# Kernel tuning notes

Measured on AMD Instinct MI355X. Metric: run time of the kernel, lower is better.

The kernel has to match this reference:

```python
import jax, jax.numpy as jnp
import numpy as np

B, N, CIN, C = 2, 400000, 192, 128
Y, X, Z = 512, 512, 40
EPS1 = 1e-5   # default BatchNorm1d eps for feature_proj
EPS2 = 1e-3   # norm_fn eps=0.001 for shared_conv BN


def setup_inputs() -> dict:
    key = jax.random.key(0)
    ks = jax.random.split(key, 12)
    voxel_features = jax.random.normal(ks[0], (N, CIN), jnp.float32)
    bi = jax.random.randint(ks[1], (N,), 0, B)
    zi = jax.random.randint(ks[2], (N,), 0, Z)
    yi = jax.random.randint(ks[3], (N,), 0, Y)
    xi = jax.random.randint(ks[4], (N,), 0, X)
    voxel_coords = jnp.stack([bi, zi, yi, xi], axis=1).astype(jnp.int32)  # (N,4)=[b,z,y,x]
    # feature_proj: Linear(CIN->C) + BN1d (inference stats) + ReLU
    W_proj = jax.random.normal(ks[5], (CIN, C), jnp.float32) * np.float32(1.0 / np.sqrt(CIN))
    b_proj = jnp.zeros((C,), jnp.float32)
    bn1_gamma = jnp.ones((C,), jnp.float32)
    bn1_beta = jnp.zeros((C,), jnp.float32)
    bn1_mean = jax.random.normal(ks[6], (C,), jnp.float32) * np.float32(0.1)
    bn1_var = jax.random.uniform(ks[7], (C,), jnp.float32, 0.5, 1.5)
    # shared_conv: SubMConv2d(C,C,3,pad=1,bias) + BN(eps=1e-3) + ReLU
    conv_w = jax.random.normal(ks[8], (3, 3, C, C), jnp.float32) * np.float32(1.0 / np.sqrt(9 * C))
    conv_b = jnp.zeros((C,), jnp.float32)
    bn2_gamma = jnp.ones((C,), jnp.float32)
    bn2_beta = jnp.zeros((C,), jnp.float32)
    bn2_mean = jax.random.normal(ks[9], (C,), jnp.float32) * np.float32(0.1)
    bn2_var = jax.random.uniform(ks[10], (C,), jnp.float32, 0.5, 1.5)
    return dict(voxel_features=voxel_features, voxel_coords=voxel_coords,
                W_proj=W_proj, b_proj=b_proj,
                bn1_gamma=bn1_gamma, bn1_beta=bn1_beta, bn1_mean=bn1_mean, bn1_var=bn1_var,
                conv_w=conv_w, conv_b=conv_b,
                bn2_gamma=bn2_gamma, bn2_beta=bn2_beta, bn2_mean=bn2_mean, bn2_var=bn2_var)


def reference(voxel_features, voxel_coords, W_proj, b_proj,
              bn1_gamma, bn1_beta, bn1_mean, bn1_var,
              conv_w, conv_b, bn2_gamma, bn2_beta, bn2_mean, bn2_var):
    # 1) feature_proj (Linear + BN1d inference + ReLU)
    f = voxel_features @ W_proj + b_proj                      # (N, C)
    f = (f - bn1_mean) * jax.lax.rsqrt(bn1_var + EPS1) * bn1_gamma + bn1_beta
    f = jax.nn.relu(f)
    # 2) bev_aggregate: unique([b,y,x]) + index_add == scatter-sum to dense BEV grid
    bi, yi, xi = voxel_coords[:, 0], voxel_coords[:, 2], voxel_coords[:, 3]
    dense = jnp.zeros((B, Y, X, C), f.dtype).at[bi, yi, xi].add(f)
    active = jnp.zeros((B, Y, X), bool).at[bi, yi, xi].set(True)
    # 3) SubMConv2d(3x3, pad=1) + BN + ReLU; subm == dense conv masked to active sites
    out = jax.lax.conv_general_dilated(dense, conv_w, (1, 1), 'SAME',
                                       dimension_numbers=('NHWC', 'HWIO', 'NHWC')) + conv_b
    out = (out - bn2_mean) * jax.lax.rsqrt(bn2_var + EPS2) * bn2_gamma + bn2_beta
    out = jax.nn.relu(out)
    # sparse tensor only holds active sites; zero elsewhere
    return jnp.where(active[..., None], out, jnp.float32(0.0))  # (B, Y, X, C)
```

## Files before the change

### kernel.cpp

```cpp
#include <hip/hip_runtime.h>

#define Bq 2
#define Yq 512
#define Xq 512
#define NVOX 400000

typedef __bf16 bf16x8 __attribute__((ext_vector_type(8)));
typedef float f32x4 __attribute__((ext_vector_type(4)));
typedef float f32x16 __attribute__((ext_vector_type(16)));
typedef short s16x8 __attribute__((ext_vector_type(8)));
typedef short s16x2 __attribute__((ext_vector_type(2)));

__device__ __forceinline__ short f2bf_s(float f){
    return __builtin_bit_cast(short, static_cast<__bf16>(f));
}

__device__ __forceinline__ void atomic_pk_add_bf16(short* addr, unsigned data){
#if __has_builtin(__builtin_amdgcn_global_atomic_fadd_v2bf16)
    s16x2 v; v[0] = (short)(data & 0xffff); v[1] = (short)(data >> 16);
    __builtin_amdgcn_global_atomic_fadd_v2bf16(
        (__attribute__((address_space(1))) s16x2*)addr, v);
#else
    asm volatile("global_atomic_pk_add_bf16 %0, %1, off"
                 :: "v"(addr), "v"(data) : "memory");
#endif
}

__global__ void kprep(const float* __restrict__ conv_w, const float* __restrict__ W_proj,
                      short* __restrict__ wR, short* __restrict__ wpT){
    int tid = blockIdx.x*256 + threadIdx.x;
    if (tid < 9*128*128){
        int tap = tid >> 14; int r = tid & 16383; int co = r >> 7; int ci = r & 127;
        int nn = co >> 5, l31 = co & 31;
        int kcc = ci >> 4, hi = (ci >> 3) & 1, j = ci & 7;
        wR[(size_t)tap*16384 + nn*4096 + kcc*512 + (hi*32 + l31)*8 + j] =
            f2bf_s(conv_w[tap*16384 + ci*128 + co]);
    }
    int e = tid - 9*128*128;
    if (e >= 0 && e < 128*192){
        int co = e / 192; int ci = e - co*192;
        wpT[e] = f2bf_s(W_proj[ci*128 + co]);
    }
}

__global__ void kcount(const int* __restrict__ vc, unsigned* __restrict__ cnt,
                       unsigned char* __restrict__ act){
    int i = blockIdx.x*256 + threadIdx.x;
    if (i >= NVOX) return;
    const int4 c = *reinterpret_cast<const int4*>(vc + i*4);
    int cell = (c.x*Yq + c.z)*Xq + c.w;
    act[cell] = 1;
    atomicAdd(&cnt[cell], 1u);
}

__global__ void __launch_bounds__(256, 2)
kproj(const float* __restrict__ vf, const int* __restrict__ vc,
      const unsigned* __restrict__ cnt,
      const short* __restrict__ wpT, const float* __restrict__ bp,
      const float* __restrict__ g1, const float* __restrict__ be1,
      const float* __restrict__ mu1, const float* __restrict__ va1,
      short* __restrict__ dbf){
    __shared__ char smem[64*200*2];
    __shared__ int cellsPk[64];
    short*    A  = (short*)smem;
    unsigned* st = (unsigned*)smem;
    const int t = threadIdx.x;
    const int v0 = blockIdx.x * 64;

    const float4* vf4 = reinterpret_cast<const float4*>(vf);
    #pragma unroll
    for (int j = 0; j < 12; ++j){
        int i = t + j*256;
        int v = i / 48, kq = i - v*48;
        float4 x = vf4[(size_t)(v0 + v)*48 + kq];
        short4 s; s.x=f2bf_s(x.x); s.y=f2bf_s(x.y); s.z=f2bf_s(x.z); s.w=f2bf_s(x.w);
        *reinterpret_cast<short4*>(&A[v*200 + kq*4]) = s;
    }
    if (t < 64){
        int vi = v0 + t;
        int bi = vc[vi*4 + 0], yi = vc[vi*4 + 2], xi = vc[vi*4 + 3];
        unsigned cn = cnt[(bi*Yq + yi)*Xq + xi];
        int P = (bi*514 + (yi + 1))*514 + (xi + 1);
        cellsPk[t] = (P*8 + ((xi + 1) & 7)) | ((cn > 1) ? (1 << 30) : 0);
    }
    __syncthreads();

    const int w  = t >> 6;
    const int l  = t & 63;
    const int lr = l & 15;
    const int q  = l >> 4;

    const short* wp_lane = wpT + (size_t)(w*32 + lr)*192 + q*8;
    bf16x8 bb[2][6];
    #pragma unroll
    for (int n = 0; n < 2; ++n)
        #pragma unroll
        for (int kc = 0; kc < 6; ++kc)
            bb[n][kc] = *reinterpret_cast<const bf16x8*>(wp_lane + n*16*192 + kc*32);

    f32x4 acc[4][2] = {};
    #pragma unroll
    for (int kc = 0; kc < 6; ++kc){
        bf16x8 a[4];
        #pragma unroll
        for (int m = 0; m < 4; ++m)
            a[m] = *reinterpret_cast<const bf16x8*>(&A[(m*16 + lr)*200 + kc*32 + q*8]);
        #pragma unroll
        for (int m = 0; m < 4; ++m)
            #pragma unroll
            for (int n = 0; n < 2; ++n)
                acc[m][n] = __builtin_amdgcn_mfma_f32_16x16x32_bf16(a[m], bb[n][kc], acc[m][n], 0, 0, 0);
    }

    __syncthreads();
    const int odd = lr & 1;
    #pragma unroll
    for (int n = 0; n < 2; ++n){
        int c = w*32 + n*16 + lr;
        float s1  = g1[c] * rsqrtf(va1[c] + 1e-5f);
        float sh1 = be1[c] + (bp[c] - mu1[c]) * s1;
        int jj = w*16 + n*8 + (lr >> 1);
        #pragma unroll
        for (int m = 0; m < 4; ++m){
            #pragma unroll
            for (int r = 0; r < 4; ++r){
                int vx = m*16 + q*4 + r;
                float val = fmaxf(fmaf(acc[m][n][r], s1, sh1), 0.f);
                float vp  = __shfl_xor(val, 1);
                if (!odd){
                    unsigned data = (unsigned)(unsigned short)f2bf_s(val)
                                  | ((unsigned)(unsigned short)f2bf_s(vp) << 16);
                    st[vx*68 + jj] = data;
                }
            }
        }
    }
    __syncthreads();

    unsigned* dbf_u32 = reinterpret_cast<unsigned*>(dbf);
    #pragma unroll
    for (int i = 0; i < 16; ++i){
        int vv = w*16 + i;
        int pk = cellsPk[vv];
        int multi = pk >> 30;
        int P = (pk & 0x3fffffff) >> 3, xp7 = pk & 7;
        unsigned data = st[vv*68 + l];
        size_t idx = (size_t)P*64 + (((l >> 2) ^ xp7) << 2) + (l & 3);
        if (multi){
            if (data) atomic_pk_add_bf16((short*)(dbf_u32 + idx), data);
        } else {
            dbf_u32[idx] = data;
        }
    }
}

__global__ void __launch_bounds__(256, 3)
kconv(const short* __restrict__ dbf, const short* __restrict__ wR,
      const unsigned char* __restrict__ act, const float* __restrict__ cb,
      const float* __restrict__ g2, const float* __restrict__ be2,
      const float* __restrict__ mu2, const float* __restrict__ va2,
      float* __restrict__ out){
    __shared__ short Atile[3*1056*8];
    const int t = threadIdx.x;
    const int bid = (blockIdx.x & 7)*1024 + (blockIdx.x >> 3);
    const int b   = bid >> 12;
    const int rem = bid & 4095;
    const int y   = rem >> 3;
    const int x0  = (rem & 7) << 6;

    const int w   = t >> 6, l = t & 63;
    const int l31 = l & 31, hi = l >> 5;

    #pragma unroll
    for (int j = 0; j < 13; ++j){
        int S = j*256 + t;
        if (S < 3168){
            int r = S / 1056, s = S - r*1056;
            const short* gp = dbf + ((size_t)((b*514 + (y + r))*514 + x0)*16 + s)*8;
            __builtin_amdgcn_global_load_lds(
                (const __attribute__((address_space(1))) void*)gp,
                (__attribute__((address_space(3))) void*)
                    ((char*)Atile + (size_t)(j*256 + w*64)*16), 16, 0, 0);
        }
    }

    const short* wRb = wR + (size_t)w*4096 + l*8;
    bf16x8 Breg[2][8];
    #pragma unroll
    for (int kcc = 0; kcc < 8; ++kcc)
        Breg[0][kcc] = *reinterpret_cast<const bf16x8*>(wRb + kcc*512);

    __syncthreads();

    f32x16 acc[2] = {};

    #pragma unroll
    for (int tp = 0; tp < 9; ++tp){
        if (tp < 8){
            const short* wn = wRb + (size_t)(tp+1)*16384;
            #pragma unroll
            for (int kcc = 0; kcc < 8; ++kcc)
                Breg[(tp+1) & 1][kcc] = *reinterpret_cast<const bf16x8*>(wn + kcc*512);
        }
        const int ky = tp / 3, kx = tp - ky*3;
        const int p0 = l31 + kx, p1 = p0 + 32;
        const int base0 = (ky*1056 + p0*16)*8;
        const int base1 = (ky*1056 + p1*16)*8;
        const int pk7 = p0 & 7;
        #pragma unroll
        for (int kcc = 0; kcc < 8; ++kcc){
            const int ks = (kcc & 3)*2 + hi, hh = kcc >> 2;
            const int q  = ((hh*8 + ks) ^ pk7) << 3;
            bf16x8 a0 = *reinterpret_cast<const bf16x8*>(&Atile[base0 + q]);
            bf16x8 a1 = *reinterpret_cast<const bf16x8*>(&Atile[base1 + q]);
            acc[0] = __builtin_amdgcn_mfma_f32_32x32x16_bf16(a0, Breg[tp & 1][kcc], acc[0], 0, 0, 0);
            acc[1] = __builtin_amdgcn_mfma_f32_32x32x16_bf16(a1, Breg[tp & 1][kcc], acc[1], 0, 0, 0);
        }
    }

    const int c = w*32 + l31;
    const float s2  = g2[c] * rsqrtf(va2[c] + 1e-3f);
    const float sh2 = be2[c] + (cb[c] - mu2[c]) * s2;
    const size_t rowcell = (size_t)(b*Yq + y)*Xq + x0;
    #pragma unroll
    for (int mi = 0; mi < 2; ++mi){
        #pragma unroll
        for (int r = 0; r < 16; ++r){
            int pos = mi*32 + (r & 3) + ((r >> 2) << 3) + hi*4;
            size_t cell = rowcell + pos;
            float v = act[cell] ? fmaxf(fmaf(acc[mi][r], s2, sh2), 0.f) : 0.f;
            out[cell*128 + c] = v;
        }
    }
}

extern "C" void kernel_launch(void* const* d_in, const int* in_sizes, int n_in,
                              void* d_out, int out_size, void* d_ws, size_t ws_size,
                              hipStream_t stream){
    const float* vf  = (const float*)d_in[0];
    const int*   vc  = (const int*)  d_in[1];
    const float* Wp  = (const float*)d_in[2];
    const float* bp  = (const float*)d_in[3];
    const float* g1  = (const float*)d_in[4];
    const float* be1 = (const float*)d_in[5];
    const float* mu1 = (const float*)d_in[6];
    const float* va1 = (const float*)d_in[7];
    const float* cw  = (const float*)d_in[8];
    const float* cb  = (const float*)d_in[9];
    const float* g2  = (const float*)d_in[10];
    const float* be2 = (const float*)d_in[11];
    const float* mu2 = (const float*)d_in[12];
    const float* va2 = (const float*)d_in[13];
    float* out = (float*)d_out;
    char* ws = (char*)d_ws;

    if (ws_size < 138233856ull) return;
    short* dbf = (short*)ws;
    unsigned char* act = (unsigned char*)(ws + 135268352);
    short* wR  = (short*)(ws + 135792640);
    short* wpT = (short*)(ws + 136087552);
    unsigned* cnt = (unsigned*)(ws + 136136704);

    hipMemsetAsync(dbf, 0, 135268352, stream);
    hipMemsetAsync(act, 0, 524288, stream);
    hipMemsetAsync(cnt, 0, 2097152, stream);
    kprep<<<672, 256, 0, stream>>>(cw, Wp, wR, wpT);
    kcount<<<1563, 256, 0, stream>>>(vc, cnt, act);
    kproj<<<6250, 256, 0, stream>>>(vf, vc, cnt, wpT, bp, g1, be1, mu1, va1, dbf);
    kconv<<<8192, 256, 0, stream>>>(dbf, wR, act, cb, g2, be2, mu2, va2, out);
}
```

Measured before the change: 363.2 us.

## Tile conv blocks over two output rows with 2x2 MFMA per wave

Each conv block now covers two output rows by 64 columns and loads a 4-row halo tile instead of a 3-row one, which cuts redundant halo loads from the dense BEV buffer. Each wave handles one row and 64 output channels, so it computes a 2x2 grid of MFMA tiles and reuses every A fragment against two weight banks. Weight banks are double-buffered in registers, with schedule barriers separating the prefetch from the compute. The cost is more registers and LDS per block, so launch bounds drop to 2 blocks per CU, and the grid is halved.

```diff
diff --git a/kernel.cpp b/kernel.cpp
--- a/kernel.cpp
+++ b/kernel.cpp
@@ -31,9 +31,9 @@
     int tid = blockIdx.x*256 + threadIdx.x;
     if (tid < 9*128*128){
         int tap = tid >> 14; int r = tid & 16383; int co = r >> 7; int ci = r & 127;
-        int nn = co >> 5, l31 = co & 31;
+        int g = co >> 5, l31 = co & 31;
         int kcc = ci >> 4, hi = (ci >> 3) & 1, j = ci & 7;
-        wR[(size_t)tap*16384 + nn*4096 + kcc*512 + (hi*32 + l31)*8 + j] =
+        wR[(size_t)tap*16384 + g*4096 + kcc*512 + (hi*32 + l31)*8 + j] =
             f2bf_s(conv_w[tap*16384 + ci*128 + co]);
     }
     int e = tid - 9*128*128;
@@ -154,29 +154,30 @@
     }
 }
 
-__global__ void __launch_bounds__(256, 3)
+__global__ void __launch_bounds__(256, 2)
 kconv(const short* __restrict__ dbf, const short* __restrict__ wR,
       const unsigned char* __restrict__ act, const float* __restrict__ cb,
       const float* __restrict__ g2, const float* __restrict__ be2,
       const float* __restrict__ mu2, const float* __restrict__ va2,
       float* __restrict__ out){
-    __shared__ short Atile[3*1056*8];
+    __shared__ short Atile[4*1056*8];
     const int t = threadIdx.x;
-    const int bid = (blockIdx.x & 7)*1024 + (blockIdx.x >> 3);
-    const int b   = bid >> 12;
-    const int rem = bid & 4095;
-    const int y   = rem >> 3;
+    const int bid = (blockIdx.x & 7)*512 + (blockIdx.x >> 3);
+    const int b   = bid >> 11;
+    const int rem = bid & 2047;
+    const int y0  = (rem >> 3) << 1;
     const int x0  = (rem & 7) << 6;
 
     const int w   = t >> 6, l = t & 63;
+    const int yy  = w >> 1, nn = w & 1;
     const int l31 = l & 31, hi = l >> 5;
 
     #pragma unroll
-    for (int j = 0; j < 13; ++j){
+    for (int j = 0; j < 17; ++j){
         int S = j*256 + t;
-        if (S < 3168){
+        if (S < 4224){
             int r = S / 1056, s = S - r*1056;
-            const short* gp = dbf + ((size_t)((b*514 + (y + r))*514 + x0)*16 + s)*8;
+            const short* gp = dbf + ((size_t)((b*514 + (y0 + r))*514 + x0)*16 + s)*8;
             __builtin_amdgcn_global_load_lds(
                 (const __attribute__((address_space(1))) void*)gp,
                 (__attribute__((address_space(3))) void*)
@@ -184,52 +185,75 @@
         }
     }
 
-    const short* wRb = wR + (size_t)w*4096 + l*8;
-    bf16x8 Breg[2][8];
-    #pragma unroll
-    for (int kcc = 0; kcc < 8; ++kcc)
-        Breg[0][kcc] = *reinterpret_cast<const bf16x8*>(wRb + kcc*512);
-
-    __syncthreads();
-
-    f32x16 acc[2] = {};
+    const short* wR_lane = wR + (size_t)(2*nn)*4096 + l*8;
+
+    bf16x8 BrA[2][8], BrB[2][8];
+
+    #define LOADBANK(DST, TP) do {                                            \
+        const short* g0_ = wR_lane + (size_t)(TP)*16384;                      \
+        _Pragma("unroll")                                                     \
+        for (int kcc_ = 0; kcc_ < 8; ++kcc_){                                 \
+            DST[0][kcc_] = *reinterpret_cast<const bf16x8*>(g0_ + kcc_*512);  \
+            DST[1][kcc_] = *reinterpret_cast<const bf16x8*>(g0_ + 4096 + kcc_*512); \
+        }                                                                     \
+    } while(0)
+
+    #define TAPBODY(BK, TP) do {                                              \
+        const int ky_ = (TP)/3, kx_ = (TP) - ky_*3;                           \
+        const int row_ = yy + ky_;                                            \
+        const int p0_ = l31 + kx_, p1_ = p0_ + 32;                            \
+        const int b0_ = (row_*1056 + p0_*16)*8;                               \
+        const int b1_ = (row_*1056 + p1_*16)*8;                               \
+        const int pk_ = p0_ & 7;                                              \
+        _Pragma("unroll")                                                     \
+        for (int kcc_ = 0; kcc_ < 8; ++kcc_){                                 \
+            const int ks_ = (kcc_ & 3)*2 + hi, hh_ = kcc_ >> 2;               \
+            const int q_  = ((hh_*8 + ks_) ^ pk_) << 3;                       \
+            bf16x8 a0_ = *reinterpret_cast<const bf16x8*>(&Atile[b0_ + q_]);  \
+            bf16x8 a1_ = *reinterpret_cast<const bf16x8*>(&Atile[b1_ + q_]);  \
+            acc[0][0] = __builtin_amdgcn_mfma_f32_32x32x16_bf16(a0_, BK[0][kcc_], acc[0][0], 0, 0, 0); \
+            acc[0][1] = __builtin_amdgcn_mfma_f32_32x32x16_bf16(a0_, BK[1][kcc_], acc[0][1], 0, 0, 0); \
+            acc[1][0] = __builtin_amdgcn_mfma_f32_32x32x16_bf16(a1_, BK[0][kcc_], acc[1][0], 0, 0, 0); \
+            acc[1][1] = __builtin_amdgcn_mfma_f32_32x32x16_bf16(a1_, BK[1][kcc_], acc[1][1], 0, 0, 0); \
+        }                                                                     \
+    } while(0)
+
+    LOADBANK(BrA, 0);
+    __syncthreads();
+
+    f32x16 acc[2][2] = {};
 
     #pragma unroll
     for (int tp = 0; tp < 9; ++tp){
-        if (tp < 8){
-            const short* wn = wRb + (size_t)(tp+1)*16384;
+        if ((tp & 1) == 0){
+            if (tp < 8) LOADBANK(BrB, tp+1);
+            __builtin_amdgcn_sched_barrier(0);
+            TAPBODY(BrA, tp);
+        } else {
+            LOADBANK(BrA, tp+1);
+            __builtin_amdgcn_sched_barrier(0);
+            TAPBODY(BrB, tp);
+        }
+    }
+    #undef TAPBODY
+    #undef LOADBANK
+
+    const int yg = y0 + yy;
+    const size_t rowcell = (size_t)(b*Yq + yg)*Xq + x0;
+    #pragma unroll
+    for (int ni = 0; ni < 2; ++ni){
+        int c = nn*64 + ni*32 + l31;
+        float s2  = g2[c] * rsqrtf(va2[c] + 1e-3f);
+        float sh2 = be2[c] + (cb[c] - mu2[c]) * s2;
+        #pragma unroll
+        for (int mi = 0; mi < 2; ++mi){
             #pragma unroll
-            for (int kcc = 0; kcc < 8; ++kcc)
-                Breg[(tp+1) & 1][kcc] = *reinterpret_cast<const bf16x8*>(wn + kcc*512);
-        }
-        const int ky = tp / 3, kx = tp - ky*3;
-        const int p0 = l31 + kx, p1 = p0 + 32;
-        const int base0 = (ky*1056 + p0*16)*8;
-        const int base1 = (ky*1056 + p1*16)*8;
-        const int pk7 = p0 & 7;
-        #pragma unroll
-        for (int kcc = 0; kcc < 8; ++kcc){
-            const int ks = (kcc & 3)*2 + hi, hh = kcc >> 2;
-            const int q  = ((hh*8 + ks) ^ pk7) << 3;
-            bf16x8 a0 = *reinterpret_cast<const bf16x8*>(&Atile[base0 + q]);
-            bf16x8 a1 = *reinterpret_cast<const bf16x8*>(&Atile[base1 + q]);
-            acc[0] = __builtin_amdgcn_mfma_f32_32x32x16_bf16(a0, Breg[tp & 1][kcc], acc[0], 0, 0, 0);
-            acc[1] = __builtin_amdgcn_mfma_f32_32x32x16_bf16(a1, Breg[tp & 1][kcc], acc[1], 0, 0, 0);
-        }
-    }
-
-    const int c = w*32 + l31;
-    const float s2  = g2[c] * rsqrtf(va2[c] + 1e-3f);
-    const float sh2 = be2[c] + (cb[c] - mu2[c]) * s2;
-    const size_t rowcell = (size_t)(b*Yq + y)*Xq + x0;
-    #pragma unroll
-    for (int mi = 0; mi < 2; ++mi){
-        #pragma unroll
-        for (int r = 0; r < 16; ++r){
-            int pos = mi*32 + (r & 3) + ((r >> 2) << 3) + hi*4;
-            size_t cell = rowcell + pos;
-            float v = act[cell] ? fmaxf(fmaf(acc[mi][r], s2, sh2), 0.f) : 0.f;
-            out[cell*128 + c] = v;
+            for (int r = 0; r < 16; ++r){
+                int pos = mi*32 + (r & 3) + ((r >> 2) << 3) + hi*4;
+                size_t cell = rowcell + pos;
+                float v = act[cell] ? fmaxf(fmaf(acc[mi][ni][r], s2, sh2), 0.f) : 0.f;
+                out[cell*128 + c] = v;
+            }
         }
     }
 }
@@ -267,5 +291,5 @@
     kprep<<<672, 256, 0, stream>>>(cw, Wp, wR, wpT);
     kcount<<<1563, 256, 0, stream>>>(vc, cnt, act);
     kproj<<<6250, 256, 0, stream>>>(vf, vc, cnt, wpT, bp, g1, be1, mu1, va1, dbf);
-    kconv<<<8192, 256, 0, stream>>>(dbf, wR, act, cb, g2, be2, mu2, va2, out);
-}
+    kconv<<<4096, 256, 0, stream>>>(dbf, wR, act, cb, g2, be2, mu2, va2, out);
+}
```

Result: no change. 363.0 us (-0.1%).
